# Kernel tuning notes

Measured on AMD Instinct MI355X. Metric: run time of the kernel, lower is better.

Reference implementation:

```python
import jax, jax.numpy as jnp
import numpy as np

NF, B, C, H, W = 5, 8, 64, 128, 128

def setup_inputs() -> dict:
    key = jax.random.key(0)
    k1, k2, k3, k4, k5 = jax.random.split(key, 5)
    return {
        "inp": jax.random.normal(k1, (NF, B, C, H, W), dtype=jnp.float32),
        "origin_w": jax.random.normal(k2, (C, NF * C), dtype=jnp.float32) * 0.05,
        "origin_b": jax.random.normal(k3, (C,), dtype=jnp.float32) * 0.05,
        "out_w": jax.random.normal(k4, (1, 2 * C), dtype=jnp.float32) * 0.05,
        "out_b": jax.random.normal(k5, (1,), dtype=jnp.float32) * 0.05,
    }

def reference(inp, origin_w, origin_b, out_w, out_b):
    nf, b, c, h, w = inp.shape
    # concat frames along channel dim: [b, nf*c, h, w]
    x = jnp.transpose(inp, (1, 0, 2, 3, 4)).reshape(b, nf * c, h, w)
    # 1x1 conv -> origin query, viewed as [b, c, 1, h*w]
    origin = jnp.einsum('ok,bkhw->bohw', origin_w, x) + origin_b[None, :, None, None]
    origin = origin.reshape(b, c, 1, h * w)
    last = inp[-1]  # [b, c, h, w]
    # difference basis: [b, c, nf-1, h*w]
    basis = jnp.stack([last - inp[i] for i in range(nf - 1)], axis=2).reshape(b, c, nf - 1, h * w)
    # L2 normalize over the spatial (last) dim, torch F.normalize semantics (eps=1e-12)
    norm = jnp.sqrt(jnp.sum(basis * basis, axis=-1, keepdims=True))
    basis1 = basis / jnp.maximum(norm, 1e-12)
    # tiny-MN batched matmuls: [b,c,1,hw] x [b,c,hw,nf-1] -> [b,c,1,nf-1]
    score = jnp.einsum('bcik,bcjk->bcij', origin, basis1)
    # [b,c,1,nf-1] x [b,c,nf-1,hw] -> [b,c,1,hw]; original views back as (b,c,w,h)
    out = jnp.einsum('bcij,bcjk->bcik', score, basis1).reshape(b, c, w, h)
    cat = jnp.concatenate([out, last], axis=1)  # [b, 2c, h, w]
    y = jnp.einsum('ok,bkhw->bohw', out_w, cat) + out_b[None, :, None, None]
    return y
```

## Files before the change

kernel.cpp:

```cpp
#include <hip/hip_runtime.h>
#include <math.h>

#define NF 5
#define NB 8
#define NC 64
#define HW 16384
#define NK 320
#define FSTRIDE (NB*NC*HW)

#define EN_FLOATS    (NB*NC*8)
#define ALPHA_FLOATS (NB*NK)

#define OST2 132

__global__ void k0_wp(const float* __restrict__ W, float* __restrict__ Wp){
    int idx = blockIdx.x*256 + threadIdx.x;
    if (idx < NC*NK){
        int c = idx / NK;
        int k = idx - c*NK;
        Wp[((c>>4)*NK + k)*16 + (c&15)] = W[idx];
    }
}

__global__ __launch_bounds__(256, 4) void k1_fused(
    const float* __restrict__ inp, const float* __restrict__ Wp,
    const float* __restrict__ bias, float* __restrict__ EN)
{
    __shared__ float Ol[64*OST2];

    const int tid = threadIdx.x;
    const int l   = tid & 63;
    const int wv  = __builtin_amdgcn_readfirstlane(tid >> 6);
    const int c0  = wv << 4;
    const int b   = blockIdx.x >> 7;
    const int s0  = (blockIdx.x & 127) << 7;

    float2 a0,a1,a2,a3,a4,a5,a6,a7,a8,a9,a10,a11,a12,a13,a14,a15;
    {
        float4 b0 = *reinterpret_cast<const float4*>(bias + c0);
        float4 b1 = *reinterpret_cast<const float4*>(bias + c0 + 4);
        float4 b2 = *reinterpret_cast<const float4*>(bias + c0 + 8);
        float4 b3 = *reinterpret_cast<const float4*>(bias + c0 + 12);
        a0  = make_float2(b0.x,b0.x); a1  = make_float2(b0.y,b0.y);
        a2  = make_float2(b0.z,b0.z); a3  = make_float2(b0.w,b0.w);
        a4  = make_float2(b1.x,b1.x); a5  = make_float2(b1.y,b1.y);
        a6  = make_float2(b1.z,b1.z); a7  = make_float2(b1.w,b1.w);
        a8  = make_float2(b2.x,b2.x); a9  = make_float2(b2.y,b2.y);
        a10 = make_float2(b2.z,b2.z); a11 = make_float2(b2.w,b2.w);
        a12 = make_float2(b3.x,b3.x); a13 = make_float2(b3.y,b3.y);
        a14 = make_float2(b3.z,b3.z); a15 = make_float2(b3.w,b3.w);
    }

    const float* wbase = Wp + (size_t)wv * NK * 16;

#define FMA2(A, WS) A.x = fmaf(WS, xv.x, A.x); A.y = fmaf(WS, xv.y, A.y);

#pragma unroll 1
    for (int f=0; f<NF; ++f){
        const float* xp = inp + (size_t)(f*NB + b)*NC*HW + s0 + (l << 1);
        const float* wf = wbase + f*64*16;
#pragma unroll 4
        for (int k=0; k<64; ++k){
            float2 xv = *reinterpret_cast<const float2*>(xp);
            xp += HW;
            const float* wk = wf + (k << 4);
            float4 w0 = *reinterpret_cast<const float4*>(wk);
            float4 w1 = *reinterpret_cast<const float4*>(wk + 4);
            float4 w2 = *reinterpret_cast<const float4*>(wk + 8);
            float4 w3 = *reinterpret_cast<const float4*>(wk + 12);
            FMA2(a0, w0.x) FMA2(a1, w0.y) FMA2(a2, w0.z) FMA2(a3, w0.w)
            FMA2(a4, w1.x) FMA2(a5, w1.y) FMA2(a6, w1.z) FMA2(a7, w1.w)
            FMA2(a8, w2.x) FMA2(a9, w2.y) FMA2(a10,w2.z) FMA2(a11,w2.w)
            FMA2(a12,w3.x) FMA2(a13,w3.y) FMA2(a14,w3.z) FMA2(a15,w3.w)
        }
    }
#undef FMA2

    {
        float* od = Ol + (size_t)c0*OST2 + (l << 1);
        *reinterpret_cast<float2*>(od +  0*OST2) = a0;
        *reinterpret_cast<float2*>(od +  1*OST2) = a1;
        *reinterpret_cast<float2*>(od +  2*OST2) = a2;
        *reinterpret_cast<float2*>(od +  3*OST2) = a3;
        *reinterpret_cast<float2*>(od +  4*OST2) = a4;
        *reinterpret_cast<float2*>(od +  5*OST2) = a5;
        *reinterpret_cast<float2*>(od +  6*OST2) = a6;
        *reinterpret_cast<float2*>(od +  7*OST2) = a7;
        *reinterpret_cast<float2*>(od +  8*OST2) = a8;
        *reinterpret_cast<float2*>(od +  9*OST2) = a9;
        *reinterpret_cast<float2*>(od + 10*OST2) = a10;
        *reinterpret_cast<float2*>(od + 11*OST2) = a11;
        *reinterpret_cast<float2*>(od + 12*OST2) = a12;
        *reinterpret_cast<float2*>(od + 13*OST2) = a13;
        *reinterpret_cast<float2*>(od + 14*OST2) = a14;
        *reinterpret_cast<float2*>(od + 15*OST2) = a15;
    }
    __syncthreads();

    const int c  = tid >> 2;
    const int ii = tid & 3;
    const float* orow = Ol + c*OST2;
    const float* x4r  = inp + (size_t)((4*NB + b)*NC + c)*HW + s0;
    const float* xir  = inp + (size_t)((ii*NB + b)*NC + c)*HW + s0;
    float e = 0.f, n = 0.f;
#pragma unroll 4
    for (int j=0; j<32; ++j){
        float4 ov = *reinterpret_cast<const float4*>(orow + (j<<2));
        float4 x4 = *reinterpret_cast<const float4*>(x4r  + (j<<2));
        float4 xi = *reinterpret_cast<const float4*>(xir  + (j<<2));
        float d0 = x4.x - xi.x, d1 = x4.y - xi.y;
        float d2 = x4.z - xi.z, d3 = x4.w - xi.w;
        n = fmaf(d0,d0, fmaf(d1,d1, fmaf(d2,d2, fmaf(d3,d3, n))));
        e = fmaf(ov.x,d0, fmaf(ov.y,d1, fmaf(ov.z,d2, fmaf(ov.w,d3, e))));
    }
    float* enb = EN + ((size_t)b*NC + c)*8;
    atomicAdd(&enb[ii],     e);
    atomicAdd(&enb[4 + ii], n);
}

__global__ void k2_coef(const float* __restrict__ EN, const float* __restrict__ out_w,
                        float* __restrict__ alpha)
{
    int tid = threadIdx.x;
    int b = tid >> 6, c = tid & 63;
    const float* e = EN + (b*NC + c)*8;
    float w1 = out_w[c], w2 = out_w[NC + c];
    float csum = 0.f;
#pragma unroll
    for (int i=0; i<4; ++i){
        float nc = fmaxf(sqrtf(e[4+i]), 1e-12f);
        float coef = e[i] / (nc*nc);
        alpha[b*NK + i*NC + c] = -w1*coef;
        csum += coef;
    }
    alpha[b*NK + 4*NC + c] = w1*csum + w2;
}

__global__ __launch_bounds__(256) void k3_out(const float* __restrict__ inp,
        const float* __restrict__ alpha, const float* __restrict__ out_b,
        float* __restrict__ y)
{
    __shared__ float  Al[80];
    __shared__ float4 P[256];
    const int tid = threadIdx.x;
    const int blk = blockIdx.x;
    const int b   = blk >> 8;
    const int sw  = (blk >> 2) & 63;
    const int rg  = blk & 3;
    const int s0  = sw << 8;
    const int sg  = tid & 63;
    const int rg2 = tid >> 6;

    if (tid < 20)
        reinterpret_cast<float4*>(Al)[tid] =
            reinterpret_cast<const float4*>(alpha + b*NK + rg*80)[tid];
    __syncthreads();

    float4 acc = make_float4(0.f, 0.f, 0.f, 0.f);
    const int rbase = rg*80 + rg2*20;
#pragma unroll 4
    for (int j=0; j<20; ++j){
        int r = rbase + j;
        const float* p = inp + (size_t)(((r>>6)*NB + b)*NC + (r&63))*HW + s0 + (sg<<2);
        float4 xv = *reinterpret_cast<const float4*>(p);
        float  w  = Al[rg2*20 + j];
        acc.x = fmaf(w, xv.x, acc.x); acc.y = fmaf(w, xv.y, acc.y);
        acc.z = fmaf(w, xv.z, acc.z); acc.w = fmaf(w, xv.w, acc.w);
    }
    P[tid] = acc;
    __syncthreads();
    if (tid < 64){
        float4 r0 = P[tid], r1 = P[tid+64], r2 = P[tid+128], r3 = P[tid+192];
        float vx = r0.x + r1.x + r2.x + r3.x;
        float vy = r0.y + r1.y + r2.y + r3.y;
        float vz = r0.z + r1.z + r2.z + r3.z;
        float vw = r0.w + r1.w + r2.w + r3.w;
        if (rg == 0){
            float bb = out_b[0];
            vx += bb; vy += bb; vz += bb; vw += bb;
        }
        float* yp = y + (size_t)b*HW + s0 + (tid << 2);
        atomicAdd(yp + 0, vx);
        atomicAdd(yp + 1, vy);
        atomicAdd(yp + 2, vz);
        atomicAdd(yp + 3, vw);
    }
}

extern "C" void kernel_launch(void* const* d_in, const int* in_sizes, int n_in,
                              void* d_out, int out_size, void* d_ws, size_t ws_size,
                              hipStream_t stream)
{
    const float* inp      = (const float*)d_in[0];
    const float* origin_w = (const float*)d_in[1];
    const float* origin_b = (const float*)d_in[2];
    const float* out_w    = (const float*)d_in[3];
    const float* out_b    = (const float*)d_in[4];
    float* y  = (float*)d_out;
    float* ws = (float*)d_ws;

    float* EN    = ws;
    float* alpha = ws + EN_FLOATS;
    float* Wp    = ws + EN_FLOATS + ALPHA_FLOATS;

    hipMemsetAsync(EN, 0, EN_FLOATS*sizeof(float), stream);
    hipMemsetAsync(y,  0, (size_t)NB*HW*sizeof(float), stream);
    k0_wp   <<<(NC*NK + 255)/256, 256, 0, stream>>>(origin_w, Wp);
    k1_fused<<<1024, 256, 0, stream>>>(inp, Wp, origin_b, EN);
    k2_coef <<<1, NB*NC, 0, stream>>>(EN, out_w, alpha);
    k3_out  <<<2048, 256, 0, stream>>>(inp, alpha, out_b, y);
}
```

Measured before the change: 313.0 us.

## Retile conv and output kernels, drop LDS staging and output atomics

The 1x1-conv kernel now gives each thread four spatial points and eight output channels per wave (512-thread blocks), and runs the projection phase straight from registers with wave shuffle reductions instead of staging the origin tile in LDS. The output kernel has each block reduce all 320 rows for one spatial tile across eight waves and write y directly, which removes the y memset and the atomic adds. The intent is fewer kernel-level atomics, less LDS traffic and fewer passes. In exchange, the blocks are larger and there are fewer of them, and there are many shuffle reductions plus per-channel atomics in k1.

```diff
diff --git a/kernel.cpp b/kernel.cpp
--- a/kernel.cpp
+++ b/kernel.cpp
@@ -11,111 +11,94 @@
 #define EN_FLOATS    (NB*NC*8)
 #define ALPHA_FLOATS (NB*NK)
 
-#define OST2 132
-
 __global__ void k0_wp(const float* __restrict__ W, float* __restrict__ Wp){
     int idx = blockIdx.x*256 + threadIdx.x;
     if (idx < NC*NK){
         int c = idx / NK;
         int k = idx - c*NK;
-        Wp[((c>>4)*NK + k)*16 + (c&15)] = W[idx];
+        Wp[((c>>3)*NK + k)*8 + (c&7)] = W[idx];
     }
 }
 
-__global__ __launch_bounds__(256, 4) void k1_fused(
+__device__ __forceinline__ float redsum64(float v){
+#pragma unroll
+    for (int m = 1; m < 64; m <<= 1) v += __shfl_xor(v, m, 64);
+    return v;
+}
+
+__global__ __launch_bounds__(512, 4) void k1_fused(
     const float* __restrict__ inp, const float* __restrict__ Wp,
     const float* __restrict__ bias, float* __restrict__ EN)
 {
-    __shared__ float Ol[64*OST2];
-
     const int tid = threadIdx.x;
     const int l   = tid & 63;
     const int wv  = __builtin_amdgcn_readfirstlane(tid >> 6);
-    const int c0  = wv << 4;
-    const int b   = blockIdx.x >> 7;
-    const int s0  = (blockIdx.x & 127) << 7;
+    const int c0  = wv << 3;
+    const int b   = blockIdx.x >> 6;
+    const int s0  = (blockIdx.x & 63) << 8;
 
-    float2 a0,a1,a2,a3,a4,a5,a6,a7,a8,a9,a10,a11,a12,a13,a14,a15;
+    float4 a0,a1,a2,a3,a4,a5,a6,a7;
     {
         float4 b0 = *reinterpret_cast<const float4*>(bias + c0);
         float4 b1 = *reinterpret_cast<const float4*>(bias + c0 + 4);
-        float4 b2 = *reinterpret_cast<const float4*>(bias + c0 + 8);
-        float4 b3 = *reinterpret_cast<const float4*>(bias + c0 + 12);
-        a0  = make_float2(b0.x,b0.x); a1  = make_float2(b0.y,b0.y);
-        a2  = make_float2(b0.z,b0.z); a3  = make_float2(b0.w,b0.w);
-        a4  = make_float2(b1.x,b1.x); a5  = make_float2(b1.y,b1.y);
-        a6  = make_float2(b1.z,b1.z); a7  = make_float2(b1.w,b1.w);
-        a8  = make_float2(b2.x,b2.x); a9  = make_float2(b2.y,b2.y);
-        a10 = make_float2(b2.z,b2.z); a11 = make_float2(b2.w,b2.w);
-        a12 = make_float2(b3.x,b3.x); a13 = make_float2(b3.y,b3.y);
-        a14 = make_float2(b3.z,b3.z); a15 = make_float2(b3.w,b3.w);
+        a0 = make_float4(b0.x,b0.x,b0.x,b0.x);
+        a1 = make_float4(b0.y,b0.y,b0.y,b0.y);
+        a2 = make_float4(b0.z,b0.z,b0.z,b0.z);
+        a3 = make_float4(b0.w,b0.w,b0.w,b0.w);
+        a4 = make_float4(b1.x,b1.x,b1.x,b1.x);
+        a5 = make_float4(b1.y,b1.y,b1.y,b1.y);
+        a6 = make_float4(b1.z,b1.z,b1.z,b1.z);
+        a7 = make_float4(b1.w,b1.w,b1.w,b1.w);
     }
 
-    const float* wbase = Wp + (size_t)wv * NK * 16;
+    const float* wbase = Wp + (size_t)wv * (NK*8);
 
-#define FMA2(A, WS) A.x = fmaf(WS, xv.x, A.x); A.y = fmaf(WS, xv.y, A.y);
+#define FMA4(A, WS) \
+    A.x = fmaf(WS, xv.x, A.x); A.y = fmaf(WS, xv.y, A.y); \
+    A.z = fmaf(WS, xv.z, A.z); A.w = fmaf(WS, xv.w, A.w);
 
 #pragma unroll 1
     for (int f=0; f<NF; ++f){
-        const float* xp = inp + (size_t)(f*NB + b)*NC*HW + s0 + (l << 1);
-        const float* wf = wbase + f*64*16;
-#pragma unroll 4
+        const float* xp = inp + (size_t)(f*NB + b)*NC*HW + s0 + (l << 2);
+        const float* wf = wbase + f*64*8;
+#pragma unroll 8
         for (int k=0; k<64; ++k){
-            float2 xv = *reinterpret_cast<const float2*>(xp);
+            float4 xv = *reinterpret_cast<const float4*>(xp);
             xp += HW;
-            const float* wk = wf + (k << 4);
+            const float* wk = wf + (k << 3);
             float4 w0 = *reinterpret_cast<const float4*>(wk);
             float4 w1 = *reinterpret_cast<const float4*>(wk + 4);
-            float4 w2 = *reinterpret_cast<const float4*>(wk + 8);
-            float4 w3 = *reinterpret_cast<const float4*>(wk + 12);
-            FMA2(a0, w0.x) FMA2(a1, w0.y) FMA2(a2, w0.z) FMA2(a3, w0.w)
-            FMA2(a4, w1.x) FMA2(a5, w1.y) FMA2(a6, w1.z) FMA2(a7, w1.w)
-            FMA2(a8, w2.x) FMA2(a9, w2.y) FMA2(a10,w2.z) FMA2(a11,w2.w)
-            FMA2(a12,w3.x) FMA2(a13,w3.y) FMA2(a14,w3.z) FMA2(a15,w3.w)
+            FMA4(a0, w0.x) FMA4(a1, w0.y) FMA4(a2, w0.z) FMA4(a3, w0.w)
+            FMA4(a4, w1.x) FMA4(a5, w1.y) FMA4(a6, w1.z) FMA4(a7, w1.w)
         }
     }
-#undef FMA2
+#undef FMA4
 
-    {
-        float* od = Ol + (size_t)c0*OST2 + (l << 1);
-        *reinterpret_cast<float2*>(od +  0*OST2) = a0;
-        *reinterpret_cast<float2*>(od +  1*OST2) = a1;
-        *reinterpret_cast<float2*>(od +  2*OST2) = a2;
-        *reinterpret_cast<float2*>(od +  3*OST2) = a3;
-        *reinterpret_cast<float2*>(od +  4*OST2) = a4;
-        *reinterpret_cast<float2*>(od +  5*OST2) = a5;
-        *reinterpret_cast<float2*>(od +  6*OST2) = a6;
-        *reinterpret_cast<float2*>(od +  7*OST2) = a7;
-        *reinterpret_cast<float2*>(od +  8*OST2) = a8;
-        *reinterpret_cast<float2*>(od +  9*OST2) = a9;
-        *reinterpret_cast<float2*>(od + 10*OST2) = a10;
-        *reinterpret_cast<float2*>(od + 11*OST2) = a11;
-        *reinterpret_cast<float2*>(od + 12*OST2) = a12;
-        *reinterpret_cast<float2*>(od + 13*OST2) = a13;
-        *reinterpret_cast<float2*>(od + 14*OST2) = a14;
-        *reinterpret_cast<float2*>(od + 15*OST2) = a15;
-    }
-    __syncthreads();
+#define PHASEB(CC, ACC) { \
+    const float* cb = inp + ((size_t)b*NC + (c0+(CC)))*HW + s0 + (l << 2); \
+    float4 x4 = *reinterpret_cast<const float4*>(cb + (size_t)4*FSTRIDE); \
+    float ev[4], nv[4]; \
+    _Pragma("unroll") \
+    for (int i=0; i<4; ++i){ \
+        float4 xi = *reinterpret_cast<const float4*>(cb + (size_t)i*FSTRIDE); \
+        float dx = x4.x - xi.x, dy = x4.y - xi.y; \
+        float dz = x4.z - xi.z, dw = x4.w - xi.w; \
+        nv[i] = fmaf(dx,dx, fmaf(dy,dy, fmaf(dz,dz, dw*dw))); \
+        ev[i] = fmaf((ACC).x,dx, fmaf((ACC).y,dy, fmaf((ACC).z,dz, (ACC).w*dw))); \
+    } \
+    _Pragma("unroll") \
+    for (int i=0; i<4; ++i){ ev[i] = redsum64(ev[i]); nv[i] = redsum64(nv[i]); } \
+    if (l == 0){ \
+        float* p = EN + ((size_t)b*NC + c0 + (CC))*8; \
+        atomicAdd(p+0, ev[0]); atomicAdd(p+1, ev[1]); \
+        atomicAdd(p+2, ev[2]); atomicAdd(p+3, ev[3]); \
+        atomicAdd(p+4, nv[0]); atomicAdd(p+5, nv[1]); \
+        atomicAdd(p+6, nv[2]); atomicAdd(p+7, nv[3]); \
+    } }
 
-    const int c  = tid >> 2;
-    const int ii = tid & 3;
-    const float* orow = Ol + c*OST2;
-    const float* x4r  = inp + (size_t)((4*NB + b)*NC + c)*HW + s0;
-    const float* xir  = inp + (size_t)((ii*NB + b)*NC + c)*HW + s0;
-    float e = 0.f, n = 0.f;
-#pragma unroll 4
-    for (int j=0; j<32; ++j){
-        float4 ov = *reinterpret_cast<const float4*>(orow + (j<<2));
-        float4 x4 = *reinterpret_cast<const float4*>(x4r  + (j<<2));
-        float4 xi = *reinterpret_cast<const float4*>(xir  + (j<<2));
-        float d0 = x4.x - xi.x, d1 = x4.y - xi.y;
-        float d2 = x4.z - xi.z, d3 = x4.w - xi.w;
-        n = fmaf(d0,d0, fmaf(d1,d1, fmaf(d2,d2, fmaf(d3,d3, n))));
-        e = fmaf(ov.x,d0, fmaf(ov.y,d1, fmaf(ov.z,d2, fmaf(ov.w,d3, e))));
-    }
-    float* enb = EN + ((size_t)b*NC + c)*8;
-    atomicAdd(&enb[ii],     e);
-    atomicAdd(&enb[4 + ii], n);
+    PHASEB(0, a0) PHASEB(1, a1) PHASEB(2, a2) PHASEB(3, a3)
+    PHASEB(4, a4) PHASEB(5, a5) PHASEB(6, a6) PHASEB(7, a7)
+#undef PHASEB
 }
 
 __global__ void k2_coef(const float* __restrict__ EN, const float* __restrict__ out_w,
@@ -136,54 +119,41 @@
     alpha[b*NK + 4*NC + c] = w1*csum + w2;
 }
 
-__global__ __launch_bounds__(256) void k3_out(const float* __restrict__ inp,
+__global__ __launch_bounds__(512, 4) void k3_out(const float* __restrict__ inp,
         const float* __restrict__ alpha, const float* __restrict__ out_b,
         float* __restrict__ y)
 {
-    __shared__ float  Al[80];
-    __shared__ float4 P[256];
+    __shared__ float4 P[512];
     const int tid = threadIdx.x;
-    const int blk = blockIdx.x;
-    const int b   = blk >> 8;
-    const int sw  = (blk >> 2) & 63;
-    const int rg  = blk & 3;
-    const int s0  = sw << 8;
+    const int b   = blockIdx.x >> 6;
+    const int s0  = (blockIdx.x & 63) << 8;
     const int sg  = tid & 63;
-    const int rg2 = tid >> 6;
-
-    if (tid < 20)
-        reinterpret_cast<float4*>(Al)[tid] =
-            reinterpret_cast<const float4*>(alpha + b*NK + rg*80)[tid];
-    __syncthreads();
+    const int rg  = __builtin_amdgcn_readfirstlane(tid >> 6);
 
     float4 acc = make_float4(0.f, 0.f, 0.f, 0.f);
-    const int rbase = rg*80 + rg2*20;
-#pragma unroll 4
-    for (int j=0; j<20; ++j){
-        int r = rbase + j;
+    const float* abase = alpha + b*NK + rg*40;
+#pragma unroll 8
+    for (int j=0; j<40; ++j){
+        int r = rg*40 + j;
         const float* p = inp + (size_t)(((r>>6)*NB + b)*NC + (r&63))*HW + s0 + (sg<<2);
+        float  w  = abase[j];
         float4 xv = *reinterpret_cast<const float4*>(p);
-        float  w  = Al[rg2*20 + j];
         acc.x = fmaf(w, xv.x, acc.x); acc.y = fmaf(w, xv.y, acc.y);
         acc.z = fmaf(w, xv.z, acc.z); acc.w = fmaf(w, xv.w, acc.w);
     }
     P[tid] = acc;
     __syncthreads();
     if (tid < 64){
-        float4 r0 = P[tid], r1 = P[tid+64], r2 = P[tid+128], r3 = P[tid+192];
-        float vx = r0.x + r1.x + r2.x + r3.x;
-        float vy = r0.y + r1.y + r2.y + r3.y;
-        float vz = r0.z + r1.z + r2.z + r3.z;
-        float vw = r0.w + r1.w + r2.w + r3.w;
-        if (rg == 0){
-            float bb = out_b[0];
-            vx += bb; vy += bb; vz += bb; vw += bb;
+        float4 r0 = P[tid];
+        float vx = r0.x, vy = r0.y, vz = r0.z, vw = r0.w;
+#pragma unroll
+        for (int g=1; g<8; ++g){
+            float4 q = P[tid + (g<<6)];
+            vx += q.x; vy += q.y; vz += q.z; vw += q.w;
         }
-        float* yp = y + (size_t)b*HW + s0 + (tid << 2);
-        atomicAdd(yp + 0, vx);
-        atomicAdd(yp + 1, vy);
-        atomicAdd(yp + 2, vz);
-        atomicAdd(yp + 3, vw);
+        float bb = out_b[0];
+        float4 o = make_float4(vx+bb, vy+bb, vz+bb, vw+bb);
+        *reinterpret_cast<float4*>(y + (size_t)b*HW + s0 + (tid<<2)) = o;
     }
 }
 
@@ -204,9 +174,8 @@
     float* Wp    = ws + EN_FLOATS + ALPHA_FLOATS;
 
     hipMemsetAsync(EN, 0, EN_FLOATS*sizeof(float), stream);
-    hipMemsetAsync(y,  0, (size_t)NB*HW*sizeof(float), stream);
     k0_wp   <<<(NC*NK + 255)/256, 256, 0, stream>>>(origin_w, Wp);
-    k1_fused<<<1024, 256, 0, stream>>>(inp, Wp, origin_b, EN);
+    k1_fused<<<512, 512, 0, stream>>>(inp, Wp, origin_b, EN);
     k2_coef <<<1, NB*NC, 0, stream>>>(EN, out_w, alpha);
-    k3_out  <<<2048, 256, 0, stream>>>(inp, alpha, out_b, y);
+    k3_out  <<<512, 512, 0, stream>>>(inp, alpha, out_b, y);
 }
```

Result: slower. 330.0 us (+5.4%).
